# Performance work log

Hardware: AMD Instinct MI355X
Metric: run time of the kernel (lower is better)

## Reference

```python
import jax, jax.numpy as jnp
import numpy as np

B, S, D = 2, 512, 1024   # batch, seq, hidden_size
E, K, I = 16, 8, 1024    # num_experts, num_experts_per_tok, moe_intermediate_size
I_SH = 1024              # moe_intermediate_size * num_shared_experts
ROUTE_SCALE = 2.826


def setup_inputs() -> dict:
    key = jax.random.key(0)
    ks = jax.random.split(key, 8)
    s = 0.02
    return {
        "x": jax.random.normal(ks[0], (B, S, D), dtype=jnp.float32),
        "gate_w": jax.random.normal(ks[1], (E, D), dtype=jnp.float32) * s,
        "expert_bias": jnp.zeros((E,), dtype=jnp.float32),
        "w_gate": jax.random.normal(ks[2], (E, I, D), dtype=jnp.float32) * s,
        "w_up": jax.random.normal(ks[3], (E, I, D), dtype=jnp.float32) * s,
        "w_down": jax.random.normal(ks[4], (E, D, I), dtype=jnp.float32) * s,
        "shared_gate_w": jax.random.normal(ks[5], (I_SH, D), dtype=jnp.float32) * s,
        "shared_up_w": jax.random.normal(ks[6], (I_SH, D), dtype=jnp.float32) * s,
        "shared_down_w": jax.random.normal(ks[7], (D, I_SH), dtype=jnp.float32) * s,
    }


def reference(x, gate_w, expert_bias, w_gate, w_up, w_down,
              shared_gate_w, shared_up_w, shared_down_w):
    # --- routing (sigmoid scores, top-k, optional norm, scale) ---
    gates = jnp.einsum('bsd,ed->bse', x, gate_w)
    scores = jax.nn.sigmoid(gates.astype(jnp.float32))           # [B,S,E]
    sel_scores = scores + expert_bias
    _, inds = jax.lax.top_k(sel_scores, K)                       # [B,S,K]
    selected = jnp.take_along_axis(scores, inds, axis=-1)        # [B,S,K]
    selected = selected / selected.sum(axis=-1, keepdims=True)   # route_norm (K>1)
    selected = selected * ROUTE_SCALE
    # combine weights as dense [B,S,E]; unselected experts get weight 0,
    # which is mathematically identical to gather-dispatch-combine.
    onehot = jax.nn.one_hot(inds, E, dtype=selected.dtype)       # [B,S,K,E]
    combine = jnp.einsum('bske,bsk->bse', onehot, selected)
    # --- experts (SwitchGLU: per-expert SwiGLU MLPs) ---
    hg = jnp.einsum('bsd,eid->bsei', x, w_gate)                  # [B,S,E,I]
    hu = jnp.einsum('bsd,eid->bsei', x, w_up)
    h = jax.nn.silu(hg) * hu
    ye = jnp.einsum('bsei,edi->bsed', h, w_down)                 # [B,S,E,D]
    y = jnp.einsum('bsed,bse->bsd', ye, combine).astype(x.dtype)
    # --- shared expert MLP (SwiGLU) ---
    g = jnp.einsum('bsd,id->bsi', x, shared_gate_w)
    u = jnp.einsum('bsd,id->bsi', x, shared_up_w)
    y = y + jnp.einsum('bsi,di->bsd', jax.nn.silu(g) * u, shared_down_w)
    return y
```

## Files before the change

### kernel.cpp

```cpp
#include <hip/hip_runtime.h>
#include <hip/hip_bf16.h>


typedef __attribute__((ext_vector_type(8))) short bf16x8;
typedef __attribute__((ext_vector_type(4))) float f32x4;

#define NTOK 1024
#define DD   1024
#define II   1024
#define NE   16
#define NEXP 17
#define KSEL 8
#define RSCALE 2.826f

#define BM 128
#define BN 64
#define BK 32
#define LDA 40

#define MB (1024ull*1024ull)
#define OFF_XBF   0ull
#define OFF_H     (2ull*MB)
#define OFF_WG    (36ull*MB)
#define OFF_WU    (70ull*MB)
#define OFF_WD    (104ull*MB)
#define OFF_LIST  (138ull*MB)
#define OFF_SCALE (OFF_LIST + 4ull*NEXP*NTOK)
#define OFF_CNT   (OFF_SCALE + 4ull*NEXP*NTOK)
#define WS_NEED   (OFF_CNT + 4096ull)

__device__ __forceinline__ unsigned short f2bf(float f) {
    union { __hip_bfloat16 h; unsigned short u; } c;
    c.h = __float2bfloat16(f);
    return c.u;
}

__device__ __forceinline__ void gl2lds16(const unsigned short* g, unsigned short* l) {
    __builtin_amdgcn_global_load_lds(
        (const __attribute__((address_space(1))) void*)g,
        (__attribute__((address_space(3))) void*)l, 16, 0, 0);
}

__global__ __launch_bounds__(256) void prep_kernel(
    const float* __restrict__ x, unsigned short* __restrict__ xbf,
    int* __restrict__ list, float* __restrict__ scalebuf, int* __restrict__ count)
{
    int idx = blockIdx.x * 256 + threadIdx.x;
    float4 v = ((const float4*)x)[idx];
    ((ushort4*)xbf)[idx] = make_ushort4(f2bf(v.x), f2bf(v.y), f2bf(v.z), f2bf(v.w));
    if (idx < NTOK) { list[NE * NTOK + idx] = idx; scalebuf[NE * NTOK + idx] = 1.0f; }
    if (idx == 0) count[NE] = NTOK;
}

__global__ __launch_bounds__(256) void wconv_kernel(
    const float* __restrict__ wg, const float* __restrict__ wu, const float* __restrict__ wd,
    const float* __restrict__ sgw, const float* __restrict__ suw, const float* __restrict__ sdw,
    unsigned short* __restrict__ wgb, unsigned short* __restrict__ wub,
    unsigned short* __restrict__ wdb)
{
    size_t i4 = (size_t)blockIdx.x * 256 + threadIdx.x;
    const size_t ROUTED4 = (size_t)NE * II * DD / 4;
    int p = blockIdx.y;
    const float* rsrc = (p == 0) ? wg : (p == 1) ? wu : wd;
    const float* ssrc = (p == 0) ? sgw : (p == 1) ? suw : sdw;
    unsigned short* dst = (p == 0) ? wgb : (p == 1) ? wub : wdb;
    const float* src = (i4 < ROUTED4) ? rsrc + 4 * i4 : ssrc + 4 * (i4 - ROUTED4);
    float4 v = *(const float4*)src;
    ((ushort4*)dst)[i4] = make_ushort4(f2bf(v.x), f2bf(v.y), f2bf(v.z), f2bf(v.w));
}

__global__ __launch_bounds__(256) void route_score_kernel(
    const float* __restrict__ x, const float* __restrict__ gw,
    const float* __restrict__ bias,
    unsigned int* __restrict__ emask, float* __restrict__ tsc)
{
    int wave = threadIdx.x >> 6, lane = threadIdx.x & 63;
    int t = blockIdx.x * 4 + wave;

    const float4* xr = (const float4*)(x + (size_t)t * DD);
    float acc[NE];
#pragma unroll
    for (int e = 0; e < NE; e++) acc[e] = 0.f;
#pragma unroll
    for (int i = 0; i < DD / 64 / 4; i++) {
        float4 xv = xr[lane + 64 * i];
#pragma unroll
        for (int e = 0; e < NE; e++) {
            float4 w = ((const float4*)(gw + (size_t)e * DD))[lane + 64 * i];
            acc[e] += xv.x * w.x + xv.y * w.y + xv.z * w.z + xv.w * w.w;
        }
    }
#pragma unroll
    for (int e = 0; e < NE; e++) {
        float v = acc[e];
        for (int off = 32; off > 0; off >>= 1) v += __shfl_xor(v, off, 64);
        acc[e] = v;
    }
    if (lane == 0) {
        float sc[NE], sel[NE];
#pragma unroll
        for (int e = 0; e < NE; e++) {
            sc[e] = 1.f / (1.f + expf(-acc[e]));
            sel[e] = sc[e] + bias[e];
        }
        bool used[NE] = {};
        int inds[KSEL];
        float ssum = 0.f;
        for (int k = 0; k < KSEL; k++) {
            float best = -1e30f; int bi = 0;
            for (int e = 0; e < NE; e++)
                if (!used[e] && sel[e] > best) { best = sel[e]; bi = e; }
            used[bi] = true; inds[k] = bi; ssum += sc[bi];
        }
        float inv = RSCALE / ssum;
        unsigned int m = 0;
        for (int k = 0; k < KSEL; k++) {
            int e = inds[k];
            m |= (1u << e);
            tsc[(size_t)t * NE + e] = sc[e] * inv;
        }
        emask[t] = m;
    }
}

__global__ __launch_bounds__(1024) void build_lists_kernel(
    const unsigned int* __restrict__ emask, const float* __restrict__ tsc,
    int* __restrict__ count, int* __restrict__ list, float* __restrict__ scalebuf)
{
    int e = blockIdx.x;
    int t = threadIdx.x;
    int lane = t & 63, wave = t >> 6;
    bool sel = (emask[t] >> e) & 1u;
    unsigned long long m = __ballot(sel);
    int posw = __popcll(m & ((1ull << lane) - 1ull));
    int wtot = __popcll(m);
    __shared__ int woff[16];
    if (lane == 0) woff[wave] = wtot;
    __syncthreads();
    if (t == 0) {
        int s = 0;
#pragma unroll
        for (int w = 0; w < 16; w++) { int v = woff[w]; woff[w] = s; s += v; }
        count[e] = s;
    }
    __syncthreads();
    if (sel) {
        int pos = woff[wave] + posw;
        list[e * NTOK + pos] = t;
        scalebuf[e * NTOK + pos] = tsc[(size_t)t * NE + e];
    }
}

__global__ __launch_bounds__(256, 3) void gateup_kernel(
    const unsigned short* __restrict__ xbf,
    const unsigned short* __restrict__ wgb, const unsigned short* __restrict__ wub,
    const int* __restrict__ count, const int* __restrict__ list,
    const float* __restrict__ scalebuf, unsigned short* __restrict__ hbuf)
{
    int s = blockIdx.x;
    int xcd = s & 7, t = s >> 3;
    int g = xcd + 8 * (t >> 4);
    int e = g >> 4;
    int n0 = (g & 15) * 64;
    int m0 = (t & 15) * 64;
    int cnt = count[e];
    if (m0 >= cnt) return;
    const unsigned short* Bg = wgb + (size_t)e * II * DD;
    const unsigned short* Bu = wub + (size_t)e * II * DD;

    __shared__ __align__(16) unsigned short As[8192];
    __shared__ __align__(16) unsigned short Bgs[8192];
    __shared__ __align__(16) unsigned short Bus[8192];
    __shared__ int rowtok[64];

    int tid = threadIdx.x;
    if (tid < 64) {
        int gr = m0 + tid;
        rowtok[tid] = list[e * NTOK + ((gr < cnt) ? gr : (cnt - 1))];
    }
    __syncthreads();

    int lane = tid & 63, wave = tid >> 6;
    int wm = wave & 1, wn = wave >> 1;
    int row16 = lane & 15, quad = lane >> 4;

    int rowS = (tid >> 2) & 63;
    int subS = (tid & 3) * 8;
    const unsigned short* gA  = xbf + (size_t)rowtok[rowS] * DD + subS;
    const unsigned short* gBg = Bg + (size_t)(n0 + rowS) * DD + subS;
    const unsigned short* gBu = Bu + (size_t)(n0 + rowS) * DD + subS;

    f32x4 accG[2][2], accU[2][2];
#pragma unroll
    for (int mi = 0; mi < 2; mi++)
#pragma unroll
        for (int ni = 0; ni < 2; ni++) {
            accG[mi][ni] = (f32x4){0.f, 0.f, 0.f, 0.f};
            accU[mi][ni] = (f32x4){0.f, 0.f, 0.f, 0.f};
        }

    for (int k0 = 0; k0 < DD; k0 += 128) {
#pragma unroll
        for (int q = 0; q < 4; q++) {
            gl2lds16(gA + k0 + q * 32, As + q * 2048 + wave * 512);
            gl2lds16(gBg + k0 + q * 32, Bgs + q * 2048 + wave * 512);
            gl2lds16(gBu + k0 + q * 32, Bus + q * 2048 + wave * 512);
        }
        __syncthreads();

#pragma unroll
        for (int kk = 0; kk < 4; kk++) {
            bf16x8 a[2], bg[2], bu[2];
#pragma unroll
            for (int mi = 0; mi < 2; mi++)
                a[mi] = *(const bf16x8*)(As + kk * 2048 + (wm * 32 + mi * 16 + row16) * 32 + quad * 8);
#pragma unroll
            for (int ni = 0; ni < 2; ni++) {
                bg[ni] = *(const bf16x8*)(Bgs + kk * 2048 + (wn * 32 + ni * 16 + row16) * 32 + quad * 8);
                bu[ni] = *(const bf16x8*)(Bus + kk * 2048 + (wn * 32 + ni * 16 + row16) * 32 + quad * 8);
            }
#pragma unroll
            for (int mi = 0; mi < 2; mi++)
#pragma unroll
                for (int ni = 0; ni < 2; ni++) {
                    accG[mi][ni] = __builtin_amdgcn_mfma_f32_16x16x32_bf16(a[mi], bg[ni], accG[mi][ni], 0, 0, 0);
                    accU[mi][ni] = __builtin_amdgcn_mfma_f32_16x16x32_bf16(a[mi], bu[ni], accU[mi][ni], 0, 0, 0);
                }
        }
        __syncthreads();
    }

#pragma unroll
    for (int mi = 0; mi < 2; mi++) {
        int grb = m0 + wm * 32 + mi * 16 + quad * 4;
#pragma unroll
        for (int r = 0; r < 4; r++) {
            int gr = grb + r;
            if (gr >= cnt) continue;
            float rs = scalebuf[e * NTOK + gr];
            size_t rowoff = ((size_t)e * NTOK + gr) * II + n0 + wn * 32;
#pragma unroll
            for (int ni = 0; ni < 2; ni++) {
                float g2 = accG[mi][ni][r], u = accU[mi][ni][r];
                float h = g2 / (1.f + __expf(-g2)) * u * rs;
                hbuf[rowoff + ni * 16 + row16] = f2bf(h);
            }
        }
    }
}

__global__ __launch_bounds__(256, 5) void down_kernel(
    const unsigned short* __restrict__ hbuf,
    const unsigned short* __restrict__ wdb,
    const int* __restrict__ count, const int* __restrict__ list,
    float* __restrict__ y)
{
    int s = blockIdx.x;
    int xcd = s & 7, t = s >> 3;
    int g = xcd + 8 * (t >> 4);
    int e = g >> 4;
    int n0 = (g & 15) * 64;
    int m0 = (t & 15) * 64;
    int cnt = count[e];
    if (m0 >= cnt) return;
    const unsigned short* Bp = wdb + (size_t)e * DD * II;

    __shared__ __align__(16) unsigned short As[8192];
    __shared__ __align__(16) unsigned short Bs[8192];

    int tid = threadIdx.x;
    int lane = tid & 63, wave = tid >> 6;
    int wm = wave & 1, wn = wave >> 1;
    int row16 = lane & 15, quad = lane >> 4;

    int rowS = (tid >> 2) & 63;
    int subS = (tid & 3) * 8;
    int grS = m0 + rowS;
    int idxS = (grS < cnt) ? grS : (cnt - 1);
    const unsigned short* gA = hbuf + ((size_t)e * NTOK + idxS) * II + subS;
    const unsigned short* gB = Bp + (size_t)(n0 + rowS) * II + subS;

    f32x4 acc[2][2];
#pragma unroll
    for (int mi = 0; mi < 2; mi++)
#pragma unroll
        for (int ni = 0; ni < 2; ni++) acc[mi][ni] = (f32x4){0.f, 0.f, 0.f, 0.f};

    for (int k0 = 0; k0 < II; k0 += 128) {
#pragma unroll
        for (int q = 0; q < 4; q++) {
            gl2lds16(gA + k0 + q * 32, As + q * 2048 + wave * 512);
            gl2lds16(gB + k0 + q * 32, Bs + q * 2048 + wave * 512);
        }
        __syncthreads();

#pragma unroll
        for (int kk = 0; kk < 4; kk++) {
            bf16x8 a[2], b[2];
#pragma unroll
            for (int mi = 0; mi < 2; mi++)
                a[mi] = *(const bf16x8*)(As + kk * 2048 + (wm * 32 + mi * 16 + row16) * 32 + quad * 8);
#pragma unroll
            for (int ni = 0; ni < 2; ni++)
                b[ni] = *(const bf16x8*)(Bs + kk * 2048 + (wn * 32 + ni * 16 + row16) * 32 + quad * 8);
#pragma unroll
            for (int mi = 0; mi < 2; mi++)
#pragma unroll
                for (int ni = 0; ni < 2; ni++)
                    acc[mi][ni] = __builtin_amdgcn_mfma_f32_16x16x32_bf16(a[mi], b[ni], acc[mi][ni], 0, 0, 0);
        }
        __syncthreads();
    }

#pragma unroll
    for (int mi = 0; mi < 2; mi++) {
        int grb = m0 + wm * 32 + mi * 16 + quad * 4;
#pragma unroll
        for (int r = 0; r < 4; r++) {
            int gr = grb + r;
            if (gr >= cnt) continue;
            int tk = list[e * NTOK + gr];
            float* yr = y + (size_t)tk * DD + n0 + wn * 32;
#pragma unroll
            for (int ni = 0; ni < 2; ni++)
                unsafeAtomicAdd(yr + ni * 16 + row16, acc[mi][ni][r]);
        }
    }
}

__global__ __launch_bounds__(256) void gateup_fb(
    const unsigned short* __restrict__ xbf,
    const float* __restrict__ wg, const float* __restrict__ wu,
    const float* __restrict__ sgw, const float* __restrict__ suw,
    const int* __restrict__ count, const int* __restrict__ list,
    const float* __restrict__ scalebuf, unsigned short* __restrict__ hbuf)
{
    int e = blockIdx.z;
    int cnt = count[e];
    int m0 = blockIdx.x * BM;
    if (m0 >= cnt) return;
    int n0 = blockIdx.y * BN;
    const float* Bg = (e < NE) ? wg + (size_t)e * II * DD : sgw;
    const float* Bu = (e < NE) ? wu + (size_t)e * II * DD : suw;

    __shared__ __align__(16) unsigned short As[BM * LDA];
    __shared__ __align__(16) unsigned short Bgs[BN * LDA];
    __shared__ __align__(16) unsigned short Bus[BN * LDA];
    __shared__ int rowtok[BM];

    int tid = threadIdx.x;
    if (tid < BM) {
        int gr = m0 + tid;
        rowtok[tid] = (gr < cnt) ? list[e * NTOK + gr] : -1;
    }
    __syncthreads();

    int lane = tid & 63, wave = tid >> 6;
    int wm = wave >> 1, wn = wave & 1;
    int row16 = lane & 15, quad = lane >> 4;

    f32x4 accG[4][2], accU[4][2];
#pragma unroll
    for (int mi = 0; mi < 4; mi++)
#pragma unroll
        for (int ni = 0; ni < 2; ni++) {
            accG[mi][ni] = (f32x4){0.f, 0.f, 0.f, 0.f};
            accU[mi][ni] = (f32x4){0.f, 0.f, 0.f, 0.f};
        }

    for (int k0 = 0; k0 < DD; k0 += BK) {
#pragma unroll
        for (int i = 0; i < 2; i++) {
            int c = tid + 256 * i;
            int row = c >> 2, kc = (c & 3) * 8;
            int tok = rowtok[row];
            uint4 v = (tok >= 0) ? *(const uint4*)(xbf + (size_t)tok * DD + k0 + kc)
                                 : make_uint4(0u, 0u, 0u, 0u);
            *(uint4*)(As + row * LDA + kc) = v;
        }
#pragma unroll
        for (int i = 0; i < 2; i++) {
            int c = tid + 256 * i;
            int row = c >> 3, f = (c & 7) * 4;
            float4 vg = *(const float4*)(Bg + (size_t)(n0 + row) * DD + k0 + f);
            float4 vu = *(const float4*)(Bu + (size_t)(n0 + row) * DD + k0 + f);
            *(ushort4*)(Bgs + row * LDA + f) = make_ushort4(f2bf(vg.x), f2bf(vg.y), f2bf(vg.z), f2bf(vg.w));
            *(ushort4*)(Bus + row * LDA + f) = make_ushort4(f2bf(vu.x), f2bf(vu.y), f2bf(vu.z), f2bf(vu.w));
        }
        __syncthreads();

        bf16x8 af[4], bg[2], bu[2];
#pragma unroll
        for (int mi = 0; mi < 4; mi++)
            af[mi] = *(const bf16x8*)(As + (wm * 64 + mi * 16 + row16) * LDA + quad * 8);
#pragma unroll
        for (int ni = 0; ni < 2; ni++) {
            bg[ni] = *(const bf16x8*)(Bgs + (wn * 32 + ni * 16 + row16) * LDA + quad * 8);
            bu[ni] = *(const bf16x8*)(Bus + (wn * 32 + ni * 16 + row16) * LDA + quad * 8);
        }
#pragma unroll
        for (int mi = 0; mi < 4; mi++)
#pragma unroll
            for (int ni = 0; ni < 2; ni++) {
                accG[mi][ni] = __builtin_amdgcn_mfma_f32_16x16x32_bf16(af[mi], bg[ni], accG[mi][ni], 0, 0, 0);
                accU[mi][ni] = __builtin_amdgcn_mfma_f32_16x16x32_bf16(af[mi], bu[ni], accU[mi][ni], 0, 0, 0);
            }
        __syncthreads();
    }

#pragma unroll
    for (int mi = 0; mi < 4; mi++) {
        int mbase = wm * 64 + mi * 16 + quad * 4;
#pragma unroll
        for (int r = 0; r < 4; r++) {
            int gr = m0 + mbase + r;
            if (gr >= cnt) continue;
            float rs = scalebuf[e * NTOK + gr];
            size_t rowoff = ((size_t)e * NTOK + gr) * II + n0;
#pragma unroll
            for (int ni = 0; ni < 2; ni++) {
                int n = wn * 32 + ni * 16 + row16;
                float g = accG[mi][ni][r], u = accU[mi][ni][r];
                float h = g / (1.f + __expf(-g)) * u * rs;
                hbuf[rowoff + n] = f2bf(h);
            }
        }
    }
}

__global__ __launch_bounds__(256) void down_fb(
    const unsigned short* __restrict__ hbuf,
    const float* __restrict__ wd, const float* __restrict__ sdw,
    const int* __restrict__ count, const int* __restrict__ list,
    float* __restrict__ y)
{
    int e = blockIdx.z;
    int cnt = count[e];
    int m0 = blockIdx.x * BM;
    if (m0 >= cnt) return;
    int n0 = blockIdx.y * BN;
    const float* Bp = (e < NE) ? wd + (size_t)e * DD * II : sdw;

    __shared__ __align__(16) unsigned short As[BM * LDA];
    __shared__ __align__(16) unsigned short Bs[BN * LDA];

    int tid = threadIdx.x;
    int lane = tid & 63, wave = tid >> 6;
    int wm = wave >> 1, wn = wave & 1;
    int row16 = lane & 15, quad = lane >> 4;

    f32x4 acc[4][2];
#pragma unroll
    for (int mi = 0; mi < 4; mi++)
#pragma unroll
        for (int ni = 0; ni < 2; ni++) acc[mi][ni] = (f32x4){0.f, 0.f, 0.f, 0.f};

    const unsigned short* Abase = hbuf + ((size_t)e * NTOK + m0) * II;

    for (int k0 = 0; k0 < II; k0 += BK) {
#pragma unroll
        for (int i = 0; i < 2; i++) {
            int c = tid + 256 * i;
            int row = c >> 2, kc = (c & 3) * 8;
            uint4 v = (m0 + row < cnt) ? *(const uint4*)(Abase + (size_t)row * II + k0 + kc)
                                       : make_uint4(0u, 0u, 0u, 0u);
            *(uint4*)(As + row * LDA + kc) = v;
        }
#pragma unroll
        for (int i = 0; i < 2; i++) {
            int c = tid + 256 * i;
            int row = c >> 3, f = (c & 7) * 4;
            float4 v = *(const float4*)(Bp + (size_t)(n0 + row) * II + k0 + f);
            *(ushort4*)(Bs + row * LDA + f) = make_ushort4(f2bf(v.x), f2bf(v.y), f2bf(v.z), f2bf(v.w));
        }
        __syncthreads();

        bf16x8 af[4], bf[2];
#pragma unroll
        for (int mi = 0; mi < 4; mi++)
            af[mi] = *(const bf16x8*)(As + (wm * 64 + mi * 16 + row16) * LDA + quad * 8);
#pragma unroll
        for (int ni = 0; ni < 2; ni++)
            bf[ni] = *(const bf16x8*)(Bs + (wn * 32 + ni * 16 + row16) * LDA + quad * 8);
#pragma unroll
        for (int mi = 0; mi < 4; mi++)
#pragma unroll
            for (int ni = 0; ni < 2; ni++)
                acc[mi][ni] = __builtin_amdgcn_mfma_f32_16x16x32_bf16(af[mi], bf[ni], acc[mi][ni], 0, 0, 0);
        __syncthreads();
    }

#pragma unroll
    for (int mi = 0; mi < 4; mi++) {
        int mbase = wm * 64 + mi * 16 + quad * 4;
#pragma unroll
        for (int r = 0; r < 4; r++) {
            int gr = m0 + mbase + r;
            if (gr >= cnt) continue;
            int t = list[e * NTOK + gr];
#pragma unroll
            for (int ni = 0; ni < 2; ni++) {
                int n = wn * 32 + ni * 16 + row16;
                unsafeAtomicAdd(&y[(size_t)t * DD + n0 + n], acc[mi][ni][r]);
            }
        }
    }
}

extern "C" void kernel_launch(void* const* d_in, const int* in_sizes, int n_in,
                              void* d_out, int out_size, void* d_ws, size_t ws_size,
                              hipStream_t stream)
{
    const float* x    = (const float*)d_in[0];
    const float* gw   = (const float*)d_in[1];
    const float* bias = (const float*)d_in[2];
    const float* wg   = (const float*)d_in[3];
    const float* wu   = (const float*)d_in[4];
    const float* wd   = (const float*)d_in[5];
    const float* sgw  = (const float*)d_in[6];
    const float* suw  = (const float*)d_in[7];
    const float* sdw  = (const float*)d_in[8];
    float* y = (float*)d_out;

    char* ws = (char*)d_ws;
    unsigned short* xbf  = (unsigned short*)(ws + OFF_XBF);
    unsigned short* hbuf = (unsigned short*)(ws + OFF_H);
    unsigned short* wgb  = (unsigned short*)(ws + OFF_WG);
    unsigned short* wub  = (unsigned short*)(ws + OFF_WU);
    unsigned short* wdb  = (unsigned short*)(ws + OFF_WD);
    int*   list     = (int*)(ws + OFF_LIST);
    float* scalebuf = (float*)(ws + OFF_SCALE);
    int*   count    = (int*)(ws + OFF_CNT);

    bool big = (ws_size >= WS_NEED);
    if (!big) {
        list     = (int*)(ws + 36ull * MB);
        scalebuf = (float*)(ws + 36ull * MB + 4ull * NEXP * NTOK);
        count    = (int*)(ws + 36ull * MB + 8ull * NEXP * NTOK);
    }

    unsigned int* emask = (unsigned int*)(ws + OFF_H);
    float*        tsc   = (float*)(ws + OFF_H + 4096);

    hipMemsetAsync(d_out, 0, (size_t)NTOK * DD * sizeof(float), stream);

    prep_kernel<<<dim3(NTOK * DD / 4 / 256), 256, 0, stream>>>(x, xbf, list, scalebuf, count);
    route_score_kernel<<<dim3(NTOK / 4), 256, 0, stream>>>(x, gw, bias, emask, tsc);
    build_lists_kernel<<<dim3(NE), 1024, 0, stream>>>(emask, tsc, count, list, scalebuf);

    if (big) {
        wconv_kernel<<<dim3((unsigned)((size_t)NEXP * II * DD / 4 / 256), 3), 256, 0, stream>>>(
            wg, wu, wd, sgw, suw, sdw, wgb, wub, wdb);
        gateup_kernel<<<dim3(NEXP * 16 * 16), 256, 0, stream>>>(
            xbf, wgb, wub, count, list, scalebuf, hbuf);
        down_kernel<<<dim3(NEXP * 16 * 16), 256, 0, stream>>>(
            hbuf, wdb, count, list, y);
    } else {
        gateup_fb<<<dim3(NTOK / BM, II / BN, NEXP), 256, 0, stream>>>(
            xbf, wg, wu, sgw, suw, count, list, scalebuf, hbuf);
        down_fb<<<dim3(NTOK / BM, DD / BN, NEXP), 256, 0, stream>>>(
            hbuf, wd, sdw, count, list, y);
    }
}
```

Before: 404.4 us.

## Enlarge gate-up and down MFMA tiles to 128x128 with XOR-swizzled LDS layout

Both expert GEMM kernels move from 64x64 to 128x128 output tiles per block, with each wave computing a 64x64 sub-tile (4x4 MFMA fragments). The K step drops to 64, the LDS staging layout is reorganized, and an XOR swizzle is added to cut bank conflicts. The aim is more operand reuse per global/LDS load and fewer blocks re-reading the same weights. The cost is higher register pressure (lower launch bounds occupancy) and coarser tiles that waste more work on partially filled expert rows.

New measurement: 396.1 us. 1.02x faster.

```diff
diff --git a/kernel.cpp b/kernel.cpp
--- a/kernel.cpp
+++ b/kernel.cpp
@@ -151,7 +151,7 @@
     }
 }
 
-__global__ __launch_bounds__(256, 3) void gateup_kernel(
+__global__ __launch_bounds__(256, 2) void gateup_kernel(
     const unsigned short* __restrict__ xbf,
     const unsigned short* __restrict__ wgb, const unsigned short* __restrict__ wub,
     const int* __restrict__ count, const int* __restrict__ list,
@@ -159,10 +159,10 @@
 {
     int s = blockIdx.x;
     int xcd = s & 7, t = s >> 3;
-    int g = xcd + 8 * (t >> 4);
-    int e = g >> 4;
-    int n0 = (g & 15) * 64;
-    int m0 = (t & 15) * 64;
+    int g = xcd + 8 * (t >> 3);
+    int e = g >> 3;
+    int n0 = (g & 7) * 128;
+    int m0 = (t & 7) * 128;
     int cnt = count[e];
     if (m0 >= cnt) return;
     const unsigned short* Bg = wgb + (size_t)e * II * DD;
@@ -171,10 +171,10 @@
     __shared__ __align__(16) unsigned short As[8192];
     __shared__ __align__(16) unsigned short Bgs[8192];
     __shared__ __align__(16) unsigned short Bus[8192];
-    __shared__ int rowtok[64];
+    __shared__ int rowtok[128];
 
     int tid = threadIdx.x;
-    if (tid < 64) {
+    if (tid < 128) {
         int gr = m0 + tid;
         rowtok[tid] = list[e * NTOK + ((gr < cnt) ? gr : (cnt - 1))];
     }
@@ -184,45 +184,52 @@
     int wm = wave & 1, wn = wave >> 1;
     int row16 = lane & 15, quad = lane >> 4;
 
-    int rowS = (tid >> 2) & 63;
-    int subS = (tid & 3) * 8;
-    const unsigned short* gA  = xbf + (size_t)rowtok[rowS] * DD + subS;
-    const unsigned short* gBg = Bg + (size_t)(n0 + rowS) * DD + subS;
-    const unsigned short* gBu = Bu + (size_t)(n0 + rowS) * DD + subS;
-
-    f32x4 accG[2][2], accU[2][2];
-#pragma unroll
-    for (int mi = 0; mi < 2; mi++)
-#pragma unroll
-        for (int ni = 0; ni < 2; ni++) {
+    int qS = wave >> 1;
+    int srow = (wave & 1) * 64 + (lane >> 2);
+    int colS = ((lane & 3) ^ ((lane >> 3) & 3)) * 8;
+    int tokr[4];
+#pragma unroll
+    for (int c = 0; c < 4; c++) tokr[c] = rowtok[srow + c * 16];
+    const unsigned short* gBg0 = Bg + (size_t)(n0 + srow) * DD + colS;
+    const unsigned short* gBu0 = Bu + (size_t)(n0 + srow) * DD + colS;
+
+    f32x4 accG[4][4], accU[4][4];
+#pragma unroll
+    for (int mi = 0; mi < 4; mi++)
+#pragma unroll
+        for (int ni = 0; ni < 4; ni++) {
             accG[mi][ni] = (f32x4){0.f, 0.f, 0.f, 0.f};
             accU[mi][ni] = (f32x4){0.f, 0.f, 0.f, 0.f};
         }
 
-    for (int k0 = 0; k0 < DD; k0 += 128) {
-#pragma unroll
-        for (int q = 0; q < 4; q++) {
-            gl2lds16(gA + k0 + q * 32, As + q * 2048 + wave * 512);
-            gl2lds16(gBg + k0 + q * 32, Bgs + q * 2048 + wave * 512);
-            gl2lds16(gBu + k0 + q * 32, Bus + q * 2048 + wave * 512);
-        }
-        __syncthreads();
-
-#pragma unroll
-        for (int kk = 0; kk < 4; kk++) {
-            bf16x8 a[2], bg[2], bu[2];
-#pragma unroll
-            for (int mi = 0; mi < 2; mi++)
-                a[mi] = *(const bf16x8*)(As + kk * 2048 + (wm * 32 + mi * 16 + row16) * 32 + quad * 8);
-#pragma unroll
-            for (int ni = 0; ni < 2; ni++) {
-                bg[ni] = *(const bf16x8*)(Bgs + kk * 2048 + (wn * 32 + ni * 16 + row16) * 32 + quad * 8);
-                bu[ni] = *(const bf16x8*)(Bus + kk * 2048 + (wn * 32 + ni * 16 + row16) * 32 + quad * 8);
+    int qe = (quad ^ ((row16 >> 1) & 3)) * 8;
+
+    for (int k0 = 0; k0 < DD; k0 += 64) {
+        int koff = k0 + qS * 32;
+#pragma unroll
+        for (int c = 0; c < 4; c++) {
+            gl2lds16(xbf + (size_t)tokr[c] * DD + koff + colS, As + wave * 2048 + c * 512);
+            gl2lds16(gBg0 + (size_t)(c * 16) * DD + koff, Bgs + wave * 2048 + c * 512);
+            gl2lds16(gBu0 + (size_t)(c * 16) * DD + koff, Bus + wave * 2048 + c * 512);
+        }
+        __syncthreads();
+
+#pragma unroll
+        for (int kk = 0; kk < 2; kk++) {
+            bf16x8 a[4], bg[4], bu[4];
+            int base = kk * 4096 + qe;
+#pragma unroll
+            for (int mi = 0; mi < 4; mi++)
+                a[mi] = *(const bf16x8*)(As + base + (wm * 64 + mi * 16 + row16) * 32);
+#pragma unroll
+            for (int ni = 0; ni < 4; ni++) {
+                bg[ni] = *(const bf16x8*)(Bgs + base + (wn * 64 + ni * 16 + row16) * 32);
+                bu[ni] = *(const bf16x8*)(Bus + base + (wn * 64 + ni * 16 + row16) * 32);
             }
 #pragma unroll
-            for (int mi = 0; mi < 2; mi++)
-#pragma unroll
-                for (int ni = 0; ni < 2; ni++) {
+            for (int mi = 0; mi < 4; mi++)
+#pragma unroll
+                for (int ni = 0; ni < 4; ni++) {
                     accG[mi][ni] = __builtin_amdgcn_mfma_f32_16x16x32_bf16(a[mi], bg[ni], accG[mi][ni], 0, 0, 0);
                     accU[mi][ni] = __builtin_amdgcn_mfma_f32_16x16x32_bf16(a[mi], bu[ni], accU[mi][ni], 0, 0, 0);
                 }
@@ -231,16 +238,16 @@
     }
 
 #pragma unroll
-    for (int mi = 0; mi < 2; mi++) {
-        int grb = m0 + wm * 32 + mi * 16 + quad * 4;
+    for (int mi = 0; mi < 4; mi++) {
+        int grb = m0 + wm * 64 + mi * 16 + quad * 4;
 #pragma unroll
         for (int r = 0; r < 4; r++) {
             int gr = grb + r;
             if (gr >= cnt) continue;
             float rs = scalebuf[e * NTOK + gr];
-            size_t rowoff = ((size_t)e * NTOK + gr) * II + n0 + wn * 32;
-#pragma unroll
-            for (int ni = 0; ni < 2; ni++) {
+            size_t rowoff = ((size_t)e * NTOK + gr) * II + n0 + wn * 64;
+#pragma unroll
+            for (int ni = 0; ni < 4; ni++) {
                 float g2 = accG[mi][ni][r], u = accU[mi][ni][r];
                 float h = g2 / (1.f + __expf(-g2)) * u * rs;
                 hbuf[rowoff + ni * 16 + row16] = f2bf(h);
@@ -249,7 +256,7 @@
     }
 }
 
-__global__ __launch_bounds__(256, 5) void down_kernel(
+__global__ __launch_bounds__(256, 3) void down_kernel(
     const unsigned short* __restrict__ hbuf,
     const unsigned short* __restrict__ wdb,
     const int* __restrict__ count, const int* __restrict__ list,
@@ -257,10 +264,10 @@
 {
     int s = blockIdx.x;
     int xcd = s & 7, t = s >> 3;
-    int g = xcd + 8 * (t >> 4);
-    int e = g >> 4;
-    int n0 = (g & 15) * 64;
-    int m0 = (t & 15) * 64;
+    int g = xcd + 8 * (t >> 3);
+    int e = g >> 3;
+    int n0 = (g & 7) * 128;
+    int m0 = (t & 7) * 128;
     int cnt = count[e];
     if (m0 >= cnt) return;
     const unsigned short* Bp = wdb + (size_t)e * DD * II;
@@ -273,56 +280,66 @@
     int wm = wave & 1, wn = wave >> 1;
     int row16 = lane & 15, quad = lane >> 4;
 
-    int rowS = (tid >> 2) & 63;
-    int subS = (tid & 3) * 8;
-    int grS = m0 + rowS;
-    int idxS = (grS < cnt) ? grS : (cnt - 1);
-    const unsigned short* gA = hbuf + ((size_t)e * NTOK + idxS) * II + subS;
-    const unsigned short* gB = Bp + (size_t)(n0 + rowS) * II + subS;
-
-    f32x4 acc[2][2];
-#pragma unroll
-    for (int mi = 0; mi < 2; mi++)
-#pragma unroll
-        for (int ni = 0; ni < 2; ni++) acc[mi][ni] = (f32x4){0.f, 0.f, 0.f, 0.f};
-
-    for (int k0 = 0; k0 < II; k0 += 128) {
-#pragma unroll
-        for (int q = 0; q < 4; q++) {
-            gl2lds16(gA + k0 + q * 32, As + q * 2048 + wave * 512);
-            gl2lds16(gB + k0 + q * 32, Bs + q * 2048 + wave * 512);
-        }
-        __syncthreads();
-
-#pragma unroll
-        for (int kk = 0; kk < 4; kk++) {
-            bf16x8 a[2], b[2];
-#pragma unroll
-            for (int mi = 0; mi < 2; mi++)
-                a[mi] = *(const bf16x8*)(As + kk * 2048 + (wm * 32 + mi * 16 + row16) * 32 + quad * 8);
-#pragma unroll
-            for (int ni = 0; ni < 2; ni++)
-                b[ni] = *(const bf16x8*)(Bs + kk * 2048 + (wn * 32 + ni * 16 + row16) * 32 + quad * 8);
-#pragma unroll
-            for (int mi = 0; mi < 2; mi++)
-#pragma unroll
-                for (int ni = 0; ni < 2; ni++)
+    int qS = wave >> 1;
+    int srow = (wave & 1) * 64 + (lane >> 2);
+    int colS = ((lane & 3) ^ ((lane >> 3) & 3)) * 8;
+
+    size_t arow[4];
+#pragma unroll
+    for (int c = 0; c < 4; c++) {
+        int gr = m0 + srow + c * 16;
+        int idx = (gr < cnt) ? gr : (cnt - 1);
+        arow[c] = ((size_t)e * NTOK + idx) * II;
+    }
+    const unsigned short* gB0 = Bp + (size_t)(n0 + srow) * II + colS;
+
+    f32x4 acc[4][4];
+#pragma unroll
+    for (int mi = 0; mi < 4; mi++)
+#pragma unroll
+        for (int ni = 0; ni < 4; ni++) acc[mi][ni] = (f32x4){0.f, 0.f, 0.f, 0.f};
+
+    int qe = (quad ^ ((row16 >> 1) & 3)) * 8;
+
+    for (int k0 = 0; k0 < II; k0 += 64) {
+        int koff = k0 + qS * 32;
+#pragma unroll
+        for (int c = 0; c < 4; c++) {
+            gl2lds16(hbuf + arow[c] + koff + colS, As + wave * 2048 + c * 512);
+            gl2lds16(gB0 + (size_t)(c * 16) * II + koff, Bs + wave * 2048 + c * 512);
+        }
+        __syncthreads();
+
+#pragma unroll
+        for (int kk = 0; kk < 2; kk++) {
+            bf16x8 a[4], b[4];
+            int base = kk * 4096 + qe;
+#pragma unroll
+            for (int mi = 0; mi < 4; mi++)
+                a[mi] = *(const bf16x8*)(As + base + (wm * 64 + mi * 16 + row16) * 32);
+#pragma unroll
+            for (int ni = 0; ni < 4; ni++)
+                b[ni] = *(const bf16x8*)(Bs + base + (wn * 64 + ni * 16 + row16) * 32);
+#pragma unroll
+            for (int mi = 0; mi < 4; mi++)
+#pragma unroll
+                for (int ni = 0; ni < 4; ni++)
                     acc[mi][ni] = __builtin_amdgcn_mfma_f32_16x16x32_bf16(a[mi], b[ni], acc[mi][ni], 0, 0, 0);
         }
         __syncthreads();
     }
 
 #pragma unroll
-    for (int mi = 0; mi < 2; mi++) {
-        int grb = m0 + wm * 32 + mi * 16 + quad * 4;
+    for (int mi = 0; mi < 4; mi++) {
+        int grb = m0 + wm * 64 + mi * 16 + quad * 4;
 #pragma unroll
         for (int r = 0; r < 4; r++) {
             int gr = grb + r;
             if (gr >= cnt) continue;
             int tk = list[e * NTOK + gr];
-            float* yr = y + (size_t)tk * DD + n0 + wn * 32;
-#pragma unroll
-            for (int ni = 0; ni < 2; ni++)
+            float* yr = y + (size_t)tk * DD + n0 + wn * 64;
+#pragma unroll
+            for (int ni = 0; ni < 4; ni++)
                 unsafeAtomicAdd(yr + ni * 16 + row16, acc[mi][ni][r]);
         }
     }
@@ -551,9 +568,9 @@
     if (big) {
         wconv_kernel<<<dim3((unsigned)((size_t)NEXP * II * DD / 4 / 256), 3), 256, 0, stream>>>(
             wg, wu, wd, sgw, suw, sdw, wgb, wub, wdb);
-        gateup_kernel<<<dim3(NEXP * 16 * 16), 256, 0, stream>>>(
+        gateup_kernel<<<dim3(NEXP * 8 * 8), 256, 0, stream>>>(
             xbf, wgb, wub, count, list, scalebuf, hbuf);
-        down_kernel<<<dim3(NEXP * 16 * 16), 256, 0, stream>>>(
+        down_kernel<<<dim3(NEXP * 8 * 8), 256, 0, stream>>>(
             hbuf, wdb, count, list, y);
     } else {
         gateup_fb<<<dim3(NTOK / BM, II / BN, NEXP), 256, 0, stream>>>(
```
